# Kernel tuning notes

Hardware: AMD Instinct MI355X
Metric: run time of the kernel (lower is better)

## Reference

```python
import jax, jax.numpy as jnp
import numpy as np

N, E = 50000, 800000
IN_DIM, HEADS, OUT_DIM = 128, 4, 32
NEG_SLOPE = 0.2
EPS = 1e-16


def setup_inputs() -> dict:
    key = jax.random.key(0)
    k = jax.random.split(key, 6)
    x = jax.random.normal(k[0], (N, IN_DIM), dtype=jnp.float32)
    edge_index = jax.random.randint(k[1], (2, E), 0, N, dtype=jnp.int64)
    # xavier-uniform-ish params
    lim_w = float(np.sqrt(6.0 / (IN_DIM + HEADS * OUT_DIM)))
    W = jax.random.uniform(k[2], (HEADS * OUT_DIM, IN_DIM), minval=-lim_w, maxval=lim_w, dtype=jnp.float32)
    lim_a = float(np.sqrt(6.0 / (1 + HEADS * OUT_DIM)))
    att_src = jax.random.uniform(k[3], (1, HEADS, OUT_DIM), minval=-lim_a, maxval=lim_a, dtype=jnp.float32)
    att_dst = jax.random.uniform(k[4], (1, HEADS, OUT_DIM), minval=-lim_a, maxval=lim_a, dtype=jnp.float32)
    bias = jnp.zeros((HEADS * OUT_DIM,), dtype=jnp.float32)
    return {"x": x, "edge_index": edge_index, "W": W, "att_src": att_src, "att_dst": att_dst, "bias": bias}


def reference(x, edge_index, W, att_src, att_dst, bias):
    n = x.shape[0]
    h = (x @ W.T).reshape(n, HEADS, OUT_DIM)           # (N,H,D)
    src, dst = edge_index[0], edge_index[1]
    a_src = jnp.sum(h * att_src, axis=-1)              # (N,H)
    a_dst = jnp.sum(h * att_dst, axis=-1)              # (N,H)
    alpha = a_src[src] + a_dst[dst]                    # (E,H)
    alpha = jax.nn.leaky_relu(alpha, NEG_SLOPE)
    # segment (per-dst) softmax over edges, per head
    m = jax.ops.segment_max(alpha, dst, num_segments=n)   # (N,H)
    ex = jnp.exp(alpha - m[dst])
    s = jax.ops.segment_sum(ex, dst, num_segments=n)      # (N,H)
    alpha = ex / (s[dst] + EPS)                            # (E,H)
    # dropout p=0 (eval) -> identity
    msg = h[src] * alpha[..., None]                        # (E,H,D)
    out = jax.ops.segment_sum(msg, dst, num_segments=n)    # (N,H,D)
    out = out.reshape(n, HEADS * OUT_DIM) + bias
    alpha_pooled = alpha.mean(axis=-1)                     # (E,)
    return out, alpha_pooled
```

## Files before the change

### kernel.cpp

```cpp
#include <hip/hip_runtime.h>

#define NNODES 50000
#define NEDGES 800000
#define HD 128
#define NEG 0.2f
#define MTILE 64
#define LDW 136
#define MAXD 64
#define GEMMB ((NNODES + MTILE - 1) / MTILE)
#define NBINS 196
#define CAP 5120
#define ABLK ((NEDGES + 2047) / 2048)

typedef __attribute__((ext_vector_type(8))) short short8;
typedef __attribute__((ext_vector_type(4))) float floatx4;

static __device__ inline unsigned short f2bf(float f) {
    unsigned u = __float_as_uint(f);
    return (unsigned short)((u + 0x7FFF + ((u >> 16) & 1)) >> 16);
}
static __device__ inline float bf2f(unsigned short u) {
    return __uint_as_float(((unsigned)u) << 16);
}
static __device__ inline float lrelu_exp(float a) {
    a = (a > 0.f) ? a : NEG * a;
    return __expf(a);
}

__global__ __launch_bounds__(256, 4) void gat_main(
    const float* __restrict__ x, const float* __restrict__ W,
    const float* __restrict__ att_src, const float* __restrict__ att_dst,
    const int* __restrict__ ei,
    unsigned short* __restrict__ h, float* __restrict__ asrc,
    float* __restrict__ adst, int* __restrict__ Sg, int* __restrict__ sbuf)
{
    __shared__ __align__(16) unsigned short Wl[128 * LDW];
    const int t = threadIdx.x;

    if (blockIdx.x >= GEMMB) {
        int* hist = (int*)Wl;
        int* sh   = hist + 256;
        int* run  = sh + 256;
        int* lbuf = run + 256;
        const int blk = blockIdx.x - GEMMB;
        const int e0 = blk * 2048 + t * 8;
        const bool act = (e0 < NEDGES);
        const int cnt = (blk == ABLK - 1) ? (NEDGES - blk * 2048) : 2048;
        int4 s0 = make_int4(0, 0, 0, 0), s1 = s0, d0 = s0, d1 = s0;
        if (act) {
            s0 = *(const int4*)(ei + e0);
            s1 = *(const int4*)(ei + e0 + 4);
            d0 = *(const int4*)(ei + NEDGES + e0);
            d1 = *(const int4*)(ei + NEDGES + e0 + 4);
        }
        hist[t] = 0;
        __syncthreads();
        if (act) {
            atomicAdd(&hist[d0.x >> 8], 1); atomicAdd(&hist[d0.y >> 8], 1);
            atomicAdd(&hist[d0.z >> 8], 1); atomicAdd(&hist[d0.w >> 8], 1);
            atomicAdd(&hist[d1.x >> 8], 1); atomicAdd(&hist[d1.y >> 8], 1);
            atomicAdd(&hist[d1.z >> 8], 1); atomicAdd(&hist[d1.w >> 8], 1);
        }
        __syncthreads();
        int hv = hist[t];
        sh[t] = hv;
        __syncthreads();
        for (int off = 1; off < 256; off <<= 1) {
            int u = (t >= off) ? sh[t - off] : 0;
            __syncthreads();
            sh[t] += u;
            __syncthreads();
        }
        int ex = sh[t] - hv;
        run[t] = ex;
        Sg[blk * 257 + t] = ex;
        if (t == 0) Sg[blk * 257 + 256] = cnt;
        __syncthreads();
        if (act) {
            int ss[8] = {s0.x, s0.y, s0.z, s0.w, s1.x, s1.y, s1.z, s1.w};
            int dd[8] = {d0.x, d0.y, d0.z, d0.w, d1.x, d1.y, d1.z, d1.w};
#pragma unroll
            for (int j = 0; j < 8; j++) {
                int slot = atomicAdd(&run[dd[j] >> 8], 1);
                lbuf[slot] = ((dd[j] & 255) << 16) | ss[j];
            }
        }
        __syncthreads();
        for (int i = t; i < cnt; i += 256)
            sbuf[blk * 2048 + i] = lbuf[i];
        return;
    }

    const int rowBase = blockIdx.x * MTILE;

    for (int idx = t * 8; idx < 128 * 128; idx += 2048) {
        int r = idx >> 7, c = idx & 127;
        float4 v0 = *(const float4*)(W + idx);
        float4 v1 = *(const float4*)(W + idx + 4);
        short8 u;
        u[0] = (short)f2bf(v0.x); u[1] = (short)f2bf(v0.y);
        u[2] = (short)f2bf(v0.z); u[3] = (short)f2bf(v0.w);
        u[4] = (short)f2bf(v1.x); u[5] = (short)f2bf(v1.y);
        u[6] = (short)f2bf(v1.z); u[7] = (short)f2bf(v1.w);
        *(short8*)(Wl + r * LDW + c) = u;
    }

    const int wave = t >> 6;
    const int lane = t & 63;
    const int c16  = lane & 15;
    const int quad = lane >> 4;
    const int xr   = rowBase + wave * 16 + c16;
    short8 av[4];
#pragma unroll
    for (int kc = 0; kc < 4; kc++) {
        float4 v0 = make_float4(0.f, 0.f, 0.f, 0.f);
        float4 v1 = v0;
        if (xr < NNODES) {
            const float* p = x + (size_t)xr * 128 + kc * 32 + quad * 8;
            v0 = *(const float4*)p;
            v1 = *(const float4*)(p + 4);
        }
        short8 u;
        u[0] = (short)f2bf(v0.x); u[1] = (short)f2bf(v0.y);
        u[2] = (short)f2bf(v0.z); u[3] = (short)f2bf(v0.w);
        u[4] = (short)f2bf(v1.x); u[5] = (short)f2bf(v1.y);
        u[6] = (short)f2bf(v1.z); u[7] = (short)f2bf(v1.w);
        av[kc] = u;
    }
    __syncthreads();

    floatx4 acc[8];
#pragma unroll
    for (int nt = 0; nt < 8; nt++) acc[nt] = (floatx4)(0.f);

#pragma unroll
    for (int kc = 0; kc < 4; kc++) {
#pragma unroll
        for (int nt = 0; nt < 8; nt++) {
            short8 bv = *(const short8*)(Wl + (nt * 16 + c16) * LDW + kc * 32 + quad * 8);
            acc[nt] = __builtin_amdgcn_mfma_f32_16x16x32_bf16(av[kc], bv, acc[nt], 0, 0, 0);
        }
    }

    float As[8], Ad[8];
#pragma unroll
    for (int nt = 0; nt < 8; nt++) {
        As[nt] = att_src[nt * 16 + c16];
        Ad[nt] = att_dst[nt * 16 + c16];
    }
#pragma unroll
    for (int r = 0; r < 4; r++) {
        const int gr = rowBase + wave * 16 + quad * 4 + r;
#pragma unroll
        for (int hh = 0; hh < 4; hh++) {
            float ps = acc[2 * hh][r] * As[2 * hh] + acc[2 * hh + 1][r] * As[2 * hh + 1];
            float pd = acc[2 * hh][r] * Ad[2 * hh] + acc[2 * hh + 1][r] * Ad[2 * hh + 1];
#pragma unroll
            for (int m = 8; m >= 1; m >>= 1) {
                ps += __shfl_xor(ps, m, 64);
                pd += __shfl_xor(pd, m, 64);
            }
            if (c16 == 0 && gr < NNODES) {
                asrc[gr * 4 + hh] = ps;
                adst[gr * 4 + hh] = pd;
            }
        }
    }

    __syncthreads();
#pragma unroll
    for (int r = 0; r < 4; r++) {
        const int lr = wave * 16 + quad * 4 + r;
#pragma unroll
        for (int nt = 0; nt < 8; nt++)
            Wl[lr * LDW + nt * 16 + c16] = f2bf(acc[nt][r]);
    }
    __syncthreads();
    for (int idx = t * 8; idx < MTILE * 128; idx += 2048) {
        int r = idx >> 7, c = idx & 127;
        int g = rowBase + r;
        if (g < NNODES)
            *(short8*)(h + (size_t)g * HD + c) = *(const short8*)(Wl + r * LDW + c);
    }
}

__global__ __launch_bounds__(1024) void gat_bin(
    const int* __restrict__ Sg, const int* __restrict__ sbuf,
    int* __restrict__ coffB, int* __restrict__ coffE,
    unsigned short* __restrict__ csr)
{
    __shared__ int s0arr[391];
    __shared__ int segoff[391];
    __shared__ int ebi[CAP];
    __shared__ unsigned short ebs[CAP];
    __shared__ int hist[256], run[256], sh[512];
    const int t = threadIdx.x;
    const int b = blockIdx.x;

    int s0v = 0, lenv = 0;
    if (t < 391) {
        s0v = Sg[t * 257 + b];
        lenv = Sg[t * 257 + b + 1] - s0v;
        s0arr[t] = s0v;
    }
    if (t < 256) hist[t] = 0;
    if (t < 512) sh[t] = (t < 391) ? lenv : 0;
    __syncthreads();
    for (int off = 1; off < 512; off <<= 1) {
        int u = (t < 512 && t >= off) ? sh[t - off] : 0;
        __syncthreads();
        if (t < 512) sh[t] += u;
        __syncthreads();
    }
    if (t < 391) segoff[t] = sh[t] - lenv;
    __syncthreads();
    const int c_b = sh[390];

    for (int i = t; i < c_b; i += 1024) {
        int lo = 0, hi = 390;
        while (lo < hi) {
            int mid = (lo + hi + 1) >> 1;
            if (segoff[mid] <= i) lo = mid; else hi = mid - 1;
        }
        int e = sbuf[lo * 2048 + s0arr[lo] + (i - segoff[lo])];
        ebi[i] = e;
        atomicAdd(&hist[(e >> 16) & 255], 1);
    }
    __syncthreads();

    int hv = (t < 256) ? hist[t] : 0;
    if (t < 256) sh[t] = hv;
    __syncthreads();
    for (int off = 1; off < 256; off <<= 1) {
        int u = (t < 256 && t >= off) ? sh[t - off] : 0;
        __syncthreads();
        if (t < 256) sh[t] += u;
        __syncthreads();
    }
    if (t < 256) {
        int ex = sh[t] - hv;
        run[t] = ex;
        int n = b * 256 + t;
        if (n < NNODES) {
            coffB[n] = b * CAP + ex;
            coffE[n] = b * CAP + ex + hv;
        }
    }
    __syncthreads();

    for (int i = t; i < c_b; i += 1024) {
        int e = ebi[i];
        int slot = atomicAdd(&run[(e >> 16) & 255], 1);
        ebs[slot] = (unsigned short)(e & 0xFFFF);
    }
    __syncthreads();

    for (int i = t; i < c_b; i += 1024)
        csr[(size_t)b * CAP + i] = ebs[i];
}

__global__ __launch_bounds__(256) void gat_node(
    const int* __restrict__ coffB, const int* __restrict__ coffE,
    const unsigned short* __restrict__ csr,
    const float* __restrict__ asrc, const float* __restrict__ adst,
    const unsigned short* __restrict__ h, const float* __restrict__ bias,
    float* __restrict__ out, float* __restrict__ rsumr)
{
    __shared__ unsigned short sh_src[4 * MAXD];
    __shared__ float sh_w[4 * MAXD * 4];
    const int t = threadIdx.x;
    const int w = t >> 6;
    const int lane = t & 63;
    const int n = blockIdx.x * 4 + w;
    const int beg = coffB[n], end = coffE[n];
    const int base = w * MAXD;
    const float4 bn = *(const float4*)(adst + n * 4);

    float4 sum = make_float4(0.f, 0.f, 0.f, 0.f);
    for (int j = beg + lane; j < end; j += 64) {
        int s = csr[j];
        float4 a = *(const float4*)(asrc + s * 4);
        float4 wv;
        wv.x = lrelu_exp(a.x + bn.x);
        wv.y = lrelu_exp(a.y + bn.y);
        wv.z = lrelu_exp(a.z + bn.z);
        wv.w = lrelu_exp(a.w + bn.w);
        sum.x += wv.x; sum.y += wv.y; sum.z += wv.z; sum.w += wv.w;
        int i = j - beg;
        if (i < MAXD) {
            sh_src[base + i] = (unsigned short)s;
            *(float4*)(sh_w + (base + i) * 4) = wv;
        }
    }
#pragma unroll
    for (int m = 32; m >= 1; m >>= 1) {
        sum.x += __shfl_xor(sum.x, m, 64);
        sum.y += __shfl_xor(sum.y, m, 64);
        sum.z += __shfl_xor(sum.z, m, 64);
        sum.w += __shfl_xor(sum.w, m, 64);
    }
    float rs[4];
    rs[0] = 1.f / (sum.x + 1e-16f);
    rs[1] = 1.f / (sum.y + 1e-16f);
    rs[2] = 1.f / (sum.z + 1e-16f);
    rs[3] = 1.f / (sum.w + 1e-16f);
    if (lane == 0)
        *(float4*)(rsumr + n * 4) = make_float4(rs[0], rs[1], rs[2], rs[3]);

    const int quad = lane >> 4;
    const int i16  = lane & 15;
    const int head = i16 >> 2;
    const float rsel = rs[head];
    const int lim = (end - beg < MAXD) ? end - beg : MAXD;

    float accA[8], accB[8];
#pragma unroll
    for (int m = 0; m < 8; m++) { accA[m] = 0.f; accB[m] = 0.f; }

    int j = 0;
    for (; j + 16 <= lim; j += 16) {
        int e0 = j + quad, e1 = j + 4 + quad, e2 = j + 8 + quad, e3 = j + 12 + quad;
        int s0 = sh_src[base + e0];
        int s1 = sh_src[base + e1];
        int s2 = sh_src[base + e2];
        int s3 = sh_src[base + e3];
        float w0 = sh_w[(base + e0) * 4 + head] * rsel;
        float w1 = sh_w[(base + e1) * 4 + head] * rsel;
        float w2 = sh_w[(base + e2) * 4 + head] * rsel;
        float w3 = sh_w[(base + e3) * 4 + head] * rsel;
        short8 u0 = *(const short8*)(h + (size_t)s0 * HD + i16 * 8);
        short8 u1 = *(const short8*)(h + (size_t)s1 * HD + i16 * 8);
        short8 u2 = *(const short8*)(h + (size_t)s2 * HD + i16 * 8);
        short8 u3 = *(const short8*)(h + (size_t)s3 * HD + i16 * 8);
#pragma unroll
        for (int m = 0; m < 8; m++) {
            accA[m] = fmaf(bf2f((unsigned short)u0[m]), w0, accA[m]);
            accB[m] = fmaf(bf2f((unsigned short)u1[m]), w1, accB[m]);
            accA[m] = fmaf(bf2f((unsigned short)u2[m]), w2, accA[m]);
            accB[m] = fmaf(bf2f((unsigned short)u3[m]), w3, accB[m]);
        }
    }
    for (; j + 4 <= lim; j += 4) {
        int e0 = j + quad;
        int s0 = sh_src[base + e0];
        float w0 = sh_w[(base + e0) * 4 + head] * rsel;
        short8 u0 = *(const short8*)(h + (size_t)s0 * HD + i16 * 8);
#pragma unroll
        for (int m = 0; m < 8; m++)
            accA[m] = fmaf(bf2f((unsigned short)u0[m]), w0, accA[m]);
    }
    if (quad < lim - j) {
        int s0 = sh_src[base + j + quad];
        float w0 = sh_w[(base + j + quad) * 4 + head] * rsel;
        short8 u0 = *(const short8*)(h + (size_t)s0 * HD + i16 * 8);
#pragma unroll
        for (int m = 0; m < 8; m++)
            accA[m] = fmaf(bf2f((unsigned short)u0[m]), w0, accA[m]);
    }
    const float bnh = (head == 0) ? bn.x : (head == 1) ? bn.y
                     : (head == 2) ? bn.z : bn.w;
    for (int jj = beg + MAXD + quad; jj < end; jj += 4) {
        int s0 = csr[jj];
        float w0 = lrelu_exp(asrc[s0 * 4 + head] + bnh) * rsel;
        short8 u0 = *(const short8*)(h + (size_t)s0 * HD + i16 * 8);
#pragma unroll
        for (int m = 0; m < 8; m++)
            accA[m] = fmaf(bf2f((unsigned short)u0[m]), w0, accA[m]);
    }

#pragma unroll
    for (int m = 0; m < 8; m++) {
        accA[m] += accB[m];
        accA[m] += __shfl_xor(accA[m], 16, 64);
        accA[m] += __shfl_xor(accA[m], 32, 64);
    }
    if (quad < 2) {
        const float4 b4 = *(const float4*)(bias + i16 * 8 + quad * 4);
        float4 st;
        if (quad == 0) {
            st.x = accA[0] + b4.x; st.y = accA[1] + b4.y;
            st.z = accA[2] + b4.z; st.w = accA[3] + b4.w;
        } else {
            st.x = accA[4] + b4.x; st.y = accA[5] + b4.y;
            st.z = accA[6] + b4.z; st.w = accA[7] + b4.w;
        }
        *(float4*)(out + (size_t)n * HD + i16 * 8 + quad * 4) = st;
    }
}

static __device__ inline float apool1(
    int s, int d, const float* __restrict__ asrc,
    const float* __restrict__ adst, const float* __restrict__ rsumr)
{
    float4 a = *(const float4*)(asrc + s * 4);
    float4 b = *(const float4*)(adst + d * 4);
    float4 r = *(const float4*)(rsumr + d * 4);
    return 0.25f * (lrelu_exp(a.x + b.x) * r.x + lrelu_exp(a.y + b.y) * r.y +
                    lrelu_exp(a.z + b.z) * r.z + lrelu_exp(a.w + b.w) * r.w);
}

__global__ __launch_bounds__(256) void gat_apool(
    const int* __restrict__ ei, const float* __restrict__ asrc,
    const float* __restrict__ adst, const float* __restrict__ rsumr,
    float* __restrict__ apool)
{
    int e0 = (blockIdx.x * 256 + threadIdx.x) * 4;
    if (e0 >= NEDGES) return;
    int4 s = *(const int4*)(ei + e0);
    int4 d = *(const int4*)(ei + NEDGES + e0);
    float4 r;
    r.x = apool1(s.x, d.x, asrc, adst, rsumr);
    r.y = apool1(s.y, d.y, asrc, adst, rsumr);
    r.z = apool1(s.z, d.z, asrc, adst, rsumr);
    r.w = apool1(s.w, d.w, asrc, adst, rsumr);
    *(float4*)(apool + e0) = r;
}

extern "C" void kernel_launch(void* const* d_in, const int* in_sizes, int n_in,
                              void* d_out, int out_size, void* d_ws, size_t ws_size,
                              hipStream_t stream)
{
    const float* x       = (const float*)d_in[0];
    const int*   ei      = (const int*)d_in[1];
    const float* W       = (const float*)d_in[2];
    const float* att_src = (const float*)d_in[3];
    const float* att_dst = (const float*)d_in[4];
    const float* bias    = (const float*)d_in[5];

    float* out   = (float*)d_out;
    float* apool = out + (size_t)NNODES * HD;

    unsigned short* h = (unsigned short*)d_ws;
    float* asrc  = (float*)(h + (size_t)NNODES * HD);
    float* adst  = asrc + NNODES * 4;
    float* rsumr = adst + NNODES * 4;
    int*   Sg    = (int*)(rsumr + NNODES * 4);
    int*   coffB = Sg + ABLK * 257 + 4;
    int*   coffE = coffB + NNODES + 4;
    int*   sbuf  = coffE + NNODES + 4;
    unsigned short* csr = (unsigned short*)(sbuf + (size_t)ABLK * 2048);

    gat_main<<<GEMMB + ABLK, 256, 0, stream>>>(
        x, W, att_src, att_dst, ei, h, asrc, adst, Sg, sbuf);
    gat_bin<<<NBINS, 1024, 0, stream>>>(Sg, sbuf, coffB, coffE, csr);
    gat_node<<<NNODES / 4, 256, 0, stream>>>(
        coffB, coffE, csr, asrc, adst, h, bias, out, rsumr);
    gat_apool<<<(NEDGES / 4 + 255) / 256, 256, 0, stream>>>(
        ei, asrc, adst, rsumr, apool);
}
```

Before: 160.1 us.

## Prefetch neighbor feature rows via bpermute double-buffering in gat_node

The node aggregation kernel now loads each lane's source index once into a register and broadcasts it with ds_bpermute, so the LDS source-index array goes away. Gathers of up to 32 neighbor h rows are issued before the softmax sum is computed, and a double-buffered A/B register pipeline prefetches the next 16 rows while consuming the current ones. This hides gather latency behind the exp/reduction work. It also switches to uint4 loads with shift/mask bf16 unpacking and adds a launch-bounds occupancy hint, at the cost of higher register pressure.

```diff
diff --git a/kernel.cpp b/kernel.cpp
--- a/kernel.cpp
+++ b/kernel.cpp
@@ -18,9 +18,6 @@
 static __device__ inline unsigned short f2bf(float f) {
     unsigned u = __float_as_uint(f);
     return (unsigned short)((u + 0x7FFF + ((u >> 16) & 1)) >> 16);
-}
-static __device__ inline float bf2f(unsigned short u) {
-    return __uint_as_float(((unsigned)u) << 16);
 }
 static __device__ inline float lrelu_exp(float a) {
     a = (a > 0.f) ? a : NEG * a;
@@ -259,38 +256,82 @@
         csr[(size_t)b * CAP + i] = ebs[i];
 }
 
-__global__ __launch_bounds__(256) void gat_node(
+#define BPERM(v, idx) __builtin_amdgcn_ds_bpermute((idx) << 2, (v))
+
+#define FMA8(U, WGT, ACC) {                                              \
+    ACC[0] = fmaf(__uint_as_float((U).x << 16), WGT, ACC[0]);            \
+    ACC[1] = fmaf(__uint_as_float((U).x & 0xFFFF0000u), WGT, ACC[1]);    \
+    ACC[2] = fmaf(__uint_as_float((U).y << 16), WGT, ACC[2]);            \
+    ACC[3] = fmaf(__uint_as_float((U).y & 0xFFFF0000u), WGT, ACC[3]);    \
+    ACC[4] = fmaf(__uint_as_float((U).z << 16), WGT, ACC[4]);            \
+    ACC[5] = fmaf(__uint_as_float((U).z & 0xFFFF0000u), WGT, ACC[5]);    \
+    ACC[6] = fmaf(__uint_as_float((U).w << 16), WGT, ACC[6]);            \
+    ACC[7] = fmaf(__uint_as_float((U).w & 0xFFFF0000u), WGT, ACC[7]); }
+
+__global__ __launch_bounds__(256, 4) void gat_node(
     const int* __restrict__ coffB, const int* __restrict__ coffE,
     const unsigned short* __restrict__ csr,
     const float* __restrict__ asrc, const float* __restrict__ adst,
     const unsigned short* __restrict__ h, const float* __restrict__ bias,
     float* __restrict__ out, float* __restrict__ rsumr)
 {
-    __shared__ unsigned short sh_src[4 * MAXD];
     __shared__ float sh_w[4 * MAXD * 4];
     const int t = threadIdx.x;
     const int w = t >> 6;
     const int lane = t & 63;
     const int n = blockIdx.x * 4 + w;
     const int beg = coffB[n], end = coffE[n];
+    const int deg = end - beg;
+    const int lim = (deg < MAXD) ? deg : MAXD;
+    const int quad = lane >> 4;
+    const int i16  = lane & 15;
+    const int head = i16 >> 2;
     const int base = w * MAXD;
     const float4 bn = *(const float4*)(adst + n * 4);
 
-    float4 sum = make_float4(0.f, 0.f, 0.f, 0.f);
-    for (int j = beg + lane; j < end; j += 64) {
-        int s = csr[j];
-        float4 a = *(const float4*)(asrc + s * 4);
-        float4 wv;
+    int s_my = 0;
+    if (lane < lim) s_my = csr[beg + lane];
+
+    uint4 uA0, uA1, uA2, uA3;
+    uint4 uB0, uB1, uB2, uB3;
+    {
+        int a0 = BPERM(s_my, quad);
+        int a1 = BPERM(s_my, quad + 4);
+        int a2 = BPERM(s_my, quad + 8);
+        int a3 = BPERM(s_my, quad + 12);
+        uA0 = *(const uint4*)(h + (size_t)a0 * HD + i16 * 8);
+        uA1 = *(const uint4*)(h + (size_t)a1 * HD + i16 * 8);
+        uA2 = *(const uint4*)(h + (size_t)a2 * HD + i16 * 8);
+        uA3 = *(const uint4*)(h + (size_t)a3 * HD + i16 * 8);
+    }
+    if (lim > 16) {
+        int b0 = BPERM(s_my, quad + 16);
+        int b1 = BPERM(s_my, quad + 20);
+        int b2 = BPERM(s_my, quad + 24);
+        int b3 = BPERM(s_my, quad + 28);
+        uB0 = *(const uint4*)(h + (size_t)b0 * HD + i16 * 8);
+        uB1 = *(const uint4*)(h + (size_t)b1 * HD + i16 * 8);
+        uB2 = *(const uint4*)(h + (size_t)b2 * HD + i16 * 8);
+        uB3 = *(const uint4*)(h + (size_t)b3 * HD + i16 * 8);
+    }
+
+    float4 wv = make_float4(0.f, 0.f, 0.f, 0.f);
+    if (lane < lim) {
+        float4 a = *(const float4*)(asrc + s_my * 4);
         wv.x = lrelu_exp(a.x + bn.x);
         wv.y = lrelu_exp(a.y + bn.y);
         wv.z = lrelu_exp(a.z + bn.z);
         wv.w = lrelu_exp(a.w + bn.w);
-        sum.x += wv.x; sum.y += wv.y; sum.z += wv.z; sum.w += wv.w;
-        int i = j - beg;
-        if (i < MAXD) {
-            sh_src[base + i] = (unsigned short)s;
-            *(float4*)(sh_w + (base + i) * 4) = wv;
-        }
+        *(float4*)(sh_w + (base + lane) * 4) = wv;
+    }
+    float4 sum = wv;
+    for (int jj = beg + MAXD + lane; jj < end; jj += 64) {
+        int s = csr[jj];
+        float4 a = *(const float4*)(asrc + s * 4);
+        sum.x += lrelu_exp(a.x + bn.x);
+        sum.y += lrelu_exp(a.y + bn.y);
+        sum.z += lrelu_exp(a.z + bn.z);
+        sum.w += lrelu_exp(a.w + bn.w);
     }
 #pragma unroll
     for (int m = 32; m >= 1; m >>= 1) {
@@ -306,66 +347,51 @@
     rs[3] = 1.f / (sum.w + 1e-16f);
     if (lane == 0)
         *(float4*)(rsumr + n * 4) = make_float4(rs[0], rs[1], rs[2], rs[3]);
-
-    const int quad = lane >> 4;
-    const int i16  = lane & 15;
-    const int head = i16 >> 2;
     const float rsel = rs[head];
-    const int lim = (end - beg < MAXD) ? end - beg : MAXD;
 
     float accA[8], accB[8];
 #pragma unroll
     for (int m = 0; m < 8; m++) { accA[m] = 0.f; accB[m] = 0.f; }
 
-    int j = 0;
-    for (; j + 16 <= lim; j += 16) {
-        int e0 = j + quad, e1 = j + 4 + quad, e2 = j + 8 + quad, e3 = j + 12 + quad;
-        int s0 = sh_src[base + e0];
-        int s1 = sh_src[base + e1];
-        int s2 = sh_src[base + e2];
-        int s3 = sh_src[base + e3];
-        float w0 = sh_w[(base + e0) * 4 + head] * rsel;
-        float w1 = sh_w[(base + e1) * 4 + head] * rsel;
-        float w2 = sh_w[(base + e2) * 4 + head] * rsel;
-        float w3 = sh_w[(base + e3) * 4 + head] * rsel;
-        short8 u0 = *(const short8*)(h + (size_t)s0 * HD + i16 * 8);
-        short8 u1 = *(const short8*)(h + (size_t)s1 * HD + i16 * 8);
-        short8 u2 = *(const short8*)(h + (size_t)s2 * HD + i16 * 8);
-        short8 u3 = *(const short8*)(h + (size_t)s3 * HD + i16 * 8);
-#pragma unroll
-        for (int m = 0; m < 8; m++) {
-            accA[m] = fmaf(bf2f((unsigned short)u0[m]), w0, accA[m]);
-            accB[m] = fmaf(bf2f((unsigned short)u1[m]), w1, accB[m]);
-            accA[m] = fmaf(bf2f((unsigned short)u2[m]), w2, accA[m]);
-            accB[m] = fmaf(bf2f((unsigned short)u3[m]), w3, accB[m]);
-        }
-    }
-    for (; j + 4 <= lim; j += 4) {
-        int e0 = j + quad;
-        int s0 = sh_src[base + e0];
-        float w0 = sh_w[(base + e0) * 4 + head] * rsel;
-        short8 u0 = *(const short8*)(h + (size_t)s0 * HD + i16 * 8);
-#pragma unroll
-        for (int m = 0; m < 8; m++)
-            accA[m] = fmaf(bf2f((unsigned short)u0[m]), w0, accA[m]);
-    }
-    if (quad < lim - j) {
-        int s0 = sh_src[base + j + quad];
-        float w0 = sh_w[(base + j + quad) * 4 + head] * rsel;
-        short8 u0 = *(const short8*)(h + (size_t)s0 * HD + i16 * 8);
-#pragma unroll
-        for (int m = 0; m < 8; m++)
-            accA[m] = fmaf(bf2f((unsigned short)u0[m]), w0, accA[m]);
-    }
+#define CONSUME(U0, U1, U2, U3, J) {                                          \
+    float w0 = (J + quad      < lim) ? sh_w[(base + J + quad) * 4 + head] * rsel : 0.f;       \
+    float w1 = (J + quad + 4  < lim) ? sh_w[(base + J + quad + 4) * 4 + head] * rsel : 0.f;   \
+    float w2 = (J + quad + 8  < lim) ? sh_w[(base + J + quad + 8) * 4 + head] * rsel : 0.f;   \
+    float w3 = (J + quad + 12 < lim) ? sh_w[(base + J + quad + 12) * 4 + head] * rsel : 0.f;  \
+    FMA8(U0, w0, accA); FMA8(U1, w1, accB);                                   \
+    FMA8(U2, w2, accA); FMA8(U3, w3, accB); }
+
+#define LOADB(J, V0, V1, V2, V3) {                                            \
+    int p0 = BPERM(s_my, J + quad);                                           \
+    int p1 = BPERM(s_my, J + quad + 4);                                       \
+    int p2 = BPERM(s_my, J + quad + 8);                                       \
+    int p3 = BPERM(s_my, J + quad + 12);                                      \
+    V0 = *(const uint4*)(h + (size_t)p0 * HD + i16 * 8);                      \
+    V1 = *(const uint4*)(h + (size_t)p1 * HD + i16 * 8);                      \
+    V2 = *(const uint4*)(h + (size_t)p2 * HD + i16 * 8);                      \
+    V3 = *(const uint4*)(h + (size_t)p3 * HD + i16 * 8); }
+
+    if (lim > 0) {
+        int j = 0;
+        for (;;) {
+            CONSUME(uA0, uA1, uA2, uA3, j);
+            if (j + 32 < lim) LOADB(j + 32, uA0, uA1, uA2, uA3);
+            j += 16;
+            if (j >= lim) break;
+            CONSUME(uB0, uB1, uB2, uB3, j);
+            if (j + 32 < lim) LOADB(j + 32, uB0, uB1, uB2, uB3);
+            j += 16;
+            if (j >= lim) break;
+        }
+    }
+
     const float bnh = (head == 0) ? bn.x : (head == 1) ? bn.y
                      : (head == 2) ? bn.z : bn.w;
     for (int jj = beg + MAXD + quad; jj < end; jj += 4) {
         int s0 = csr[jj];
         float w0 = lrelu_exp(asrc[s0 * 4 + head] + bnh) * rsel;
-        short8 u0 = *(const short8*)(h + (size_t)s0 * HD + i16 * 8);
-#pragma unroll
-        for (int m = 0; m < 8; m++)
-            accA[m] = fmaf(bf2f((unsigned short)u0[m]), w0, accA[m]);
+        uint4 u = *(const uint4*)(h + (size_t)s0 * HD + i16 * 8);
+        FMA8(u, w0, accA);
     }
 
 #pragma unroll
```

Result: slower. 171.4 us (+7.1%).

## Compute softmax denominators in bin kernel instead of node kernel

Applied to the files above, without the earlier changes.

Moves the per-destination softmax sum and reciprocal out of the node kernel into the binning kernel. There, one thread per node walks its sorted edges in shared memory and gathers asrc. The node kernel now only loads the precomputed reciprocal and drops its wave-wide shuffle reduction. The cost is a serial per-thread loop in the bin kernel, so high-degree nodes cause load imbalance, and only 256 of 1024 threads do this work. Nodes with more than 64 edges still recompute weights on the fly.

```diff
diff --git a/kernel.cpp b/kernel.cpp
--- a/kernel.cpp
+++ b/kernel.cpp
@@ -186,8 +186,9 @@
 
 __global__ __launch_bounds__(1024) void gat_bin(
     const int* __restrict__ Sg, const int* __restrict__ sbuf,
+    const float* __restrict__ asrc, const float* __restrict__ adst,
     int* __restrict__ coffB, int* __restrict__ coffE,
-    unsigned short* __restrict__ csr)
+    unsigned short* __restrict__ csr, float* __restrict__ rsumr)
 {
     __shared__ int s0arr[391];
     __shared__ int segoff[391];
@@ -229,6 +230,7 @@
     __syncthreads();
 
     int hv = (t < 256) ? hist[t] : 0;
+    int ex = 0;
     if (t < 256) sh[t] = hv;
     __syncthreads();
     for (int off = 1; off < 256; off <<= 1) {
@@ -238,7 +240,7 @@
         __syncthreads();
     }
     if (t < 256) {
-        int ex = sh[t] - hv;
+        ex = sh[t] - hv;
         run[t] = ex;
         int n = b * 256 + t;
         if (n < NNODES) {
@@ -257,6 +259,28 @@
 
     for (int i = t; i < c_b; i += 1024)
         csr[(size_t)b * CAP + i] = ebs[i];
+
+    if (t < 256) {
+        int n = b * 256 + t;
+        if (n < NNODES) {
+            const float4 bn = *(const float4*)(adst + n * 4);
+            float4 s4 = make_float4(0.f, 0.f, 0.f, 0.f);
+            for (int i = ex; i < ex + hv; i++) {
+                int s = ebs[i];
+                float4 a = *(const float4*)(asrc + s * 4);
+                s4.x += lrelu_exp(a.x + bn.x);
+                s4.y += lrelu_exp(a.y + bn.y);
+                s4.z += lrelu_exp(a.z + bn.z);
+                s4.w += lrelu_exp(a.w + bn.w);
+            }
+            float4 r4;
+            r4.x = 1.f / (s4.x + 1e-16f);
+            r4.y = 1.f / (s4.y + 1e-16f);
+            r4.z = 1.f / (s4.z + 1e-16f);
+            r4.w = 1.f / (s4.w + 1e-16f);
+            *(float4*)(rsumr + n * 4) = r4;
+        }
+    }
 }
 
 __global__ __launch_bounds__(256) void gat_node(
@@ -264,7 +288,7 @@
     const unsigned short* __restrict__ csr,
     const float* __restrict__ asrc, const float* __restrict__ adst,
     const unsigned short* __restrict__ h, const float* __restrict__ bias,
-    float* __restrict__ out, float* __restrict__ rsumr)
+    float* __restrict__ out, const float* __restrict__ rsumr)
 {
     __shared__ unsigned short sh_src[4 * MAXD];
     __shared__ float sh_w[4 * MAXD * 4];
@@ -273,45 +297,30 @@
     const int lane = t & 63;
     const int n = blockIdx.x * 4 + w;
     const int beg = coffB[n], end = coffE[n];
+    const int deg = end - beg;
+    const int lim = (deg < MAXD) ? deg : MAXD;
     const int base = w * MAXD;
-    const float4 bn = *(const float4*)(adst + n * 4);
-
-    float4 sum = make_float4(0.f, 0.f, 0.f, 0.f);
-    for (int j = beg + lane; j < end; j += 64) {
-        int s = csr[j];
+
+    const float4 rs4 = *(const float4*)(rsumr + n * 4);
+
+    if (lane < lim) {
+        int s = csr[beg + lane];
+        const float4 bn = *(const float4*)(adst + n * 4);
         float4 a = *(const float4*)(asrc + s * 4);
         float4 wv;
         wv.x = lrelu_exp(a.x + bn.x);
         wv.y = lrelu_exp(a.y + bn.y);
         wv.z = lrelu_exp(a.z + bn.z);
         wv.w = lrelu_exp(a.w + bn.w);
-        sum.x += wv.x; sum.y += wv.y; sum.z += wv.z; sum.w += wv.w;
-        int i = j - beg;
-        if (i < MAXD) {
-            sh_src[base + i] = (unsigned short)s;
-            *(float4*)(sh_w + (base + i) * 4) = wv;
-        }
-    }
-#pragma unroll
-    for (int m = 32; m >= 1; m >>= 1) {
-        sum.x += __shfl_xor(sum.x, m, 64);
-        sum.y += __shfl_xor(sum.y, m, 64);
-        sum.z += __shfl_xor(sum.z, m, 64);
-        sum.w += __shfl_xor(sum.w, m, 64);
-    }
-    float rs[4];
-    rs[0] = 1.f / (sum.x + 1e-16f);
-    rs[1] = 1.f / (sum.y + 1e-16f);
-    rs[2] = 1.f / (sum.z + 1e-16f);
-    rs[3] = 1.f / (sum.w + 1e-16f);
-    if (lane == 0)
-        *(float4*)(rsumr + n * 4) = make_float4(rs[0], rs[1], rs[2], rs[3]);
+        sh_src[base + lane] = (unsigned short)s;
+        *(float4*)(sh_w + (base + lane) * 4) = wv;
+    }
 
     const int quad = lane >> 4;
     const int i16  = lane & 15;
     const int head = i16 >> 2;
-    const float rsel = rs[head];
-    const int lim = (end - beg < MAXD) ? end - beg : MAXD;
+    const float rsel = (head == 0) ? rs4.x : (head == 1) ? rs4.y
+                      : (head == 2) ? rs4.z : rs4.w;
 
     float accA[8], accB[8];
 #pragma unroll
@@ -357,15 +366,18 @@
         for (int m = 0; m < 8; m++)
             accA[m] = fmaf(bf2f((unsigned short)u0[m]), w0, accA[m]);
     }
-    const float bnh = (head == 0) ? bn.x : (head == 1) ? bn.y
-                     : (head == 2) ? bn.z : bn.w;
-    for (int jj = beg + MAXD + quad; jj < end; jj += 4) {
-        int s0 = csr[jj];
-        float w0 = lrelu_exp(asrc[s0 * 4 + head] + bnh) * rsel;
-        short8 u0 = *(const short8*)(h + (size_t)s0 * HD + i16 * 8);
-#pragma unroll
-        for (int m = 0; m < 8; m++)
-            accA[m] = fmaf(bf2f((unsigned short)u0[m]), w0, accA[m]);
+    if (deg > MAXD) {
+        const float4 bn = *(const float4*)(adst + n * 4);
+        const float bnh = (head == 0) ? bn.x : (head == 1) ? bn.y
+                         : (head == 2) ? bn.z : bn.w;
+        for (int jj = beg + MAXD + quad; jj < end; jj += 4) {
+            int s0 = csr[jj];
+            float w0 = lrelu_exp(asrc[s0 * 4 + head] + bnh) * rsel;
+            short8 u0 = *(const short8*)(h + (size_t)s0 * HD + i16 * 8);
+#pragma unroll
+            for (int m = 0; m < 8; m++)
+                accA[m] = fmaf(bf2f((unsigned short)u0[m]), w0, accA[m]);
+        }
     }
 
 #pragma unroll
@@ -442,7 +454,8 @@
 
     gat_main<<<GEMMB + ABLK, 256, 0, stream>>>(
         x, W, att_src, att_dst, ei, h, asrc, adst, Sg, sbuf);
-    gat_bin<<<NBINS, 1024, 0, stream>>>(Sg, sbuf, coffB, coffE, csr);
+    gat_bin<<<NBINS, 1024, 0, stream>>>(
+        Sg, sbuf, asrc, adst, coffB, coffE, csr, rsumr);
     gat_node<<<NNODES / 4, 256, 0, stream>>>(
         coffB, coffE, csr, asrc, adst, h, bias, out, rsumr);
     gat_apool<<<(NEDGES / 4 + 255) / 256, 256, 0, stream>>>(
```

After: 166.5 us. +4.0%, slower.
